# Kernel tuning notes

Hardware: AMD Instinct MI355X
Metric: run time of the kernel (lower is better)

## Reference

```python
import jax, jax.numpy as jnp
import numpy as np

MAX_DEG = 6

def _lookup(atoms, edges, maskvalue, include_self):
    # atoms: (B,N,F); edges: (B,N,D) with -1 padding. Shift indices by +1 and
    # prepend a mask row so padded slots read `maskvalue` (NGFP lookup_neighbors).
    B, N, F = atoms.shape
    pad = jnp.full((B, 1, F), maskvalue, atoms.dtype)
    padded = jnp.concatenate([pad, atoms], axis=1)          # (B,N+1,F)
    g = jax.vmap(lambda a, e: a[e])(padded, edges + 1)       # (B,N,D,F)
    if include_self:
        g = jnp.concatenate([atoms[:, :, None, :], g], axis=2)  # (B,N,D+1,F)
    return g

def _conv(atoms, bonds, edges, W, b):
    # Degree-specific dense layers, masked-summed (Duvenaud graph conv).
    deg = (edges != -1).sum(-1)                               # (B,N)
    summed = _lookup(atoms, edges, 0.0, True).sum(2)          # self + neighbors
    feat = jnp.concatenate([summed, bonds.sum(2)], axis=-1)   # (B,N,in)
    new = jax.nn.relu(jnp.einsum('bni,dio->bdno', feat, W) + b[None, :, None, :])
    m = (deg[:, None, :] == jnp.arange(MAX_DEG)[None, :, None]).astype(new.dtype)
    return jnp.einsum('bdno,bdn->bno', new, m)

def _pool(atoms, edges):
    nbr = _lookup(atoms, edges, -jnp.inf, True)
    mx = nbr.max(2)
    mask = ((edges != -1).sum(-1, keepdims=True) > 0).astype(atoms.dtype)
    return mx * mask

def _gout(atoms, bonds, edges, W, b):
    mask = ((edges != -1).sum(-1, keepdims=True) > 0).astype(atoms.dtype)
    feat = jnp.concatenate([atoms, bonds.sum(2)], axis=-1)
    fp = jnp.tanh(feat @ W + b) * mask
    return fp.sum(1)                                          # (B,H) graph fingerprint

def setup_inputs() -> dict:
    B, N, D = 2048, 60, MAX_DEG
    ATOM_F, BOND_F, H, C = 37, 6, 128, 12
    key = jax.random.key(0)
    ks = jax.random.split(key, 8)
    atoms = jax.random.normal(ks[0], (B, N, ATOM_F), jnp.float32)
    bonds = jax.random.uniform(ks[1], (B, N, D, BOND_F), jnp.float32)
    deg = jax.random.randint(ks[2], (B, N, 1), 1, 6)          # 1..5 neighbors per atom
    slot = jnp.arange(D)[None, None, :]
    nbrs = jax.random.randint(ks[3], (B, N, D), 0, N)
    edges = jnp.where(slot < deg, nbrs, -1)                   # -1 = padding
    s = lambda f: (2.0 / f) ** 0.5
    W1 = jax.random.normal(ks[4], (D, ATOM_F + BOND_F, H), jnp.float32) * s(ATOM_F + BOND_F)
    b1 = jnp.zeros((D, H), jnp.float32)
    W2 = jax.random.normal(ks[5], (D, H + BOND_F, H), jnp.float32) * s(H + BOND_F)
    b2 = jnp.zeros((D, H), jnp.float32)
    Wo = jax.random.normal(ks[6], (H + BOND_F, H), jnp.float32) * s(H + BOND_F)
    bo = jnp.zeros((H,), jnp.float32)
    Wfc = jax.random.normal(ks[7], (H, C), jnp.float32) * s(H)
    bfc = jnp.zeros((C,), jnp.float32)
    return dict(atoms=atoms, bonds=bonds, edges=edges, W1=W1, b1=b1,
                W2=W2, b2=b2, Wo=Wo, bo=bo, Wfc=Wfc, bfc=bfc)

def reference(atoms, bonds, edges, W1, b1, W2, b2, Wo, bo, Wfc, bfc):
    x = _conv(atoms, bonds, edges, W1, b1)   # gcn1
    x = _pool(x, edges)
    x = _conv(x, bonds, edges, W2, b2)       # gcn2
    x = _pool(x, edges)
    fp = _gout(x, bonds, edges, Wo, bo)      # graph output aggregation
    return jax.nn.sigmoid(fp @ Wfc + bfc)    # (B, n_class)
```

## Files before the change

kernel.cpp:

```cpp
#include <hip/hip_runtime.h>
#include <math.h>

typedef unsigned short u16;
typedef unsigned int   u32;
typedef unsigned long long u64;
typedef short  v8s __attribute__((ext_vector_type(8)));
typedef float  v4f __attribute__((ext_vector_type(4)));

constexpr int NB=2048, NN=60, DD=6, AF=37, BFD=6, HH=128, CC=12;
constexpr int T = 512;
constexpr int FASTR = 168;
constexpr int XSTR  = 132;
constexpr int KS1 = 2;
constexpr int KS2 = 5;
constexpr int MAXP = 32;

constexpr int W1T_UNITS = 6*8*KS1;
constexpr int W2T_UNITS = 6*8*KS2;
constexpr int WOT_UNITS = 8*KS2;
constexpr int TOT_UNITS = W1T_UNITS + W2T_UNITS + WOT_UNITS;
constexpr int W2T_OFF = W1T_UNITS*512;
constexpr int WOT_OFF = (W1T_UNITS+W2T_UNITS)*512;
constexpr int LO_OFF  = TOT_UNITS*512;

__device__ __forceinline__ u16 f2bf(float f) {
  u32 u = __float_as_uint(f);
  return (u16)((u + 0x7FFFu + ((u >> 16) & 1u)) >> 16);
}
__device__ __forceinline__ float bf2f(u16 h) { return __uint_as_float((u32)h << 16); }

__device__ __forceinline__ void split2(float a, float b, u32& hi, u32& lo) {
  u16 ha = f2bf(a), hb = f2bf(b);
  u32 la = __float_as_uint(a - bf2f(ha)) >> 16;
  u32 lb = __float_as_uint(b - bf2f(hb)) >> 16;
  hi = ((u32)hb << 16) | ha;
  lo = (lb << 16) | la;
}
__device__ __forceinline__ void split8(const float* v, uint4& hi, uint4& lo) {
  split2(v[0], v[1], hi.x, lo.x); split2(v[2], v[3], hi.y, lo.y);
  split2(v[4], v[5], hi.z, lo.z); split2(v[6], v[7], hi.w, lo.w);
}
__device__ __forceinline__ float fast_tanh(float x) {
  float e = __expf(2.f * x);
  return 1.f - 2.f / (e + 1.f);
}

__global__ __launch_bounds__(256) void prep_kernel(
    const float* __restrict__ W1, const float* __restrict__ W2,
    const float* __restrict__ Wo, u16* __restrict__ ws)
{
  int tid = blockIdx.x*256 + threadIdx.x;
  if (tid >= TOT_UNITS*512) return;
  int unit = tid >> 9, idx = tid & 511;
  int lane = idx >> 3, j = idx & 7;
  int n16 = lane & 15, q = lane >> 4;
  const float* src; int K, nt, ks;
  if (unit < W1T_UNITS) {
    int d = unit / 16, rem = unit % 16; nt = rem >> 1; ks = rem & 1;
    src = W1 + (size_t)d*43*128; K = 43;
  } else if (unit < W1T_UNITS + W2T_UNITS) {
    int u = unit - W1T_UNITS; int d = u / 40, rem = u % 40; nt = rem / 5; ks = rem % 5;
    src = W2 + (size_t)d*134*128; K = 134;
  } else {
    int u = unit - (W1T_UNITS + W2T_UNITS); nt = u / 5; ks = u % 5;
    src = Wo; K = 134;
  }
  int k = ks*32 + q*8 + j, n = nt*16 + n16;
  float v = (k < K) ? src[(size_t)k*128 + n] : 0.f;
  u16 hi = f2bf(v);
  u16 lo = (u16)(__float_as_uint(v - bf2f(hi)) >> 16);
  ws[(size_t)unit*512 + lane*8 + j] = hi;
  ws[(size_t)(LO_OFF + unit*512) + lane*8 + j] = lo;
}

template<int KSTEPS>
__device__ __forceinline__ void conv_mfma(
    const u16* __restrict__ wsW, const float* __restrict__ bias,
    const u16* sFA, float* sXout,
    const int* sSorted, const int* sDeg,
    const int* sPairD, const int* sPairM, int nP,
    int wv, int lane)
{
  const int n16 = lane & 15, q = lane >> 4;
  for (int u = wv; u < nP*4; u += 8) {
    const int p = u >> 2, nt0 = (u & 3) * 2;
    const int d = sPairD[p], mt = sPairM[p];
    const int row = mt*16 + n16;
    int nodes[4];
    #pragma unroll
    for (int r = 0; r < 4; ++r) nodes[r] = sSorted[mt*16 + q*4 + r];
    if (d == 6) {
      #pragma unroll 1
      for (int nt = nt0; nt < nt0+2; ++nt) {
        const int h = nt*16 + n16;
        #pragma unroll
        for (int r = 0; r < 4; ++r)
          if (nodes[r] >= 0 && sDeg[nodes[r]] == 6) sXout[nodes[r]*XSTR + h] = 0.f;
      }
      continue;
    }
    v8s ah[KSTEPS], al[KSTEPS];
    #pragma unroll
    for (int ks = 0; ks < KSTEPS; ++ks) {
      ah[ks] = *(const v8s*)(&sFA[row*FASTR + ks*32 + q*8]);
      al[ks] = *(const v8s*)(&sFA[(64 + row)*FASTR + ks*32 + q*8]);
    }
    #pragma unroll
    for (int nt = nt0; nt < nt0+2; ++nt) {
      v8s bh[KSTEPS], bl[KSTEPS];
      #pragma unroll
      for (int ks = 0; ks < KSTEPS; ++ks) {
        const size_t ub = ((size_t)((d*8 + nt)*KSTEPS + ks))*512;
        bh[ks] = ((const v8s*)(wsW + ub))[lane];
        bl[ks] = ((const v8s*)(wsW + LO_OFF + ub))[lane];
      }
      v4f acc = {0.f, 0.f, 0.f, 0.f};
      #pragma unroll
      for (int ks = 0; ks < KSTEPS; ++ks) {
        acc = __builtin_amdgcn_mfma_f32_16x16x32_bf16(ah[ks], bh[ks], acc, 0, 0, 0);
        acc = __builtin_amdgcn_mfma_f32_16x16x32_bf16(al[ks], bh[ks], acc, 0, 0, 0);
        acc = __builtin_amdgcn_mfma_f32_16x16x32_bf16(ah[ks], bl[ks], acc, 0, 0, 0);
      }
      const int h = nt*16 + n16;
      const float bb = bias[d*128 + h];
      #pragma unroll
      for (int r = 0; r < 4; ++r) {
        int node = nodes[r];
        if (node >= 0 && sDeg[node] == d)
          sXout[node*XSTR + h] = fmaxf(acc[r] + bb, 0.f);
      }
    }
  }
}

__global__ __launch_bounds__(T, 4) void ngfp_kernel(
    const float* __restrict__ atoms, const float* __restrict__ bonds,
    const int*   __restrict__ edges,
    const float* __restrict__ b1, const float* __restrict__ b2,
    const float* __restrict__ bo,
    const float* __restrict__ Wfc, const float* __restrict__ bfc,
    const u16*   __restrict__ ws,
    float* __restrict__ out)
{
  __shared__ u16   sFA[128*FASTR];
  __shared__ float sXa[NN*XSTR];
  __shared__ float sBsum[NN*BFD];
  __shared__ int  sEdges[NN*DD];
  __shared__ int  sDeg[NN];
  __shared__ int  sSorted[64];
  __shared__ int  sPairD[MAXP];
  __shared__ int  sPairM[MAXP];
  __shared__ int  sNP;
  __shared__ float sPart[HH];
  __shared__ float sRed[96];

  float* const sAtoms = sXa;

  const int b = blockIdx.x;
  const int t = threadIdx.x;
  const int wv = t >> 6;
  const int lane = t & 63;

  for (int i = t; i < NN*DD; i += T) sEdges[i] = edges[b*NN*DD + i];
  for (int i = t; i < NN*AF; i += T) sAtoms[i] = atoms[b*NN*AF + i];
  for (int i = t; i < NN*BFD; i += T) {
    int n = i / BFD, f = i - n*BFD;
    const float* bp = bonds + ((size_t)(b*NN + n)*DD)*BFD + f;
    float s = 0.f;
    #pragma unroll
    for (int d = 0; d < DD; ++d) s += bp[d*BFD];
    sBsum[i] = s;
  }
  __syncthreads();

  if (wv == 0) {
    const int n = lane;
    int dg = 7;
    if (n < NN) {
      dg = 0;
      #pragma unroll
      for (int d = 0; d < DD; ++d) dg += (sEdges[n*DD + d] != -1) ? 1 : 0;
      sDeg[n] = dg;
    } else {
      sSorted[n] = -1;
    }
    const u64 below = (lane == 63) ? ~0ull >> 1 : ((1ull << lane) - 1);
    int rs = 0, np = 0;
    #pragma unroll 1
    for (int d = 0; d < 7; ++d) {
      u64 m = __ballot(dg == d);
      int cnt = (int)__popcll(m);
      if (dg == d) sSorted[rs + (int)__popcll(m & below)] = n;
      if (lane == 0 && cnt > 0) {
        const int r1 = rs + cnt;
        for (int mt = rs >> 4; mt < ((r1 + 15) >> 4); ++mt) {
          sPairD[np] = d; sPairM[np] = mt; ++np;
        }
      }
      rs += cnt;
    }
    if (lane == 0) sNP = np;
  }
  __syncthreads();
  const int nP = sNP;

  {
    const int row = t >> 3, c = t & 7;
    const int node = sSorted[row];
    float acc[8] = {0,0,0,0,0,0,0,0};
    if (node >= 0) {
      int e[DD];
      #pragma unroll
      for (int d = 0; d < DD; ++d) e[d] = sEdges[node*DD + d];
      #pragma unroll
      for (int j = 0; j < 8; ++j) {
        int k = c*8 + j;
        float v = 0.f;
        if (k < AF) {
          v = sAtoms[node*AF + k];
          #pragma unroll
          for (int d = 0; d < DD; ++d) if (e[d] >= 0) v += sAtoms[e[d]*AF + k];
        } else if (k < AF + BFD) {
          v = sBsum[node*BFD + (k - AF)];
        }
        acc[j] = v;
      }
    }
    uint4 hi, lo; split8(acc, hi, lo);
    *(uint4*)(&sFA[row*FASTR + c*8]) = hi;
    *(uint4*)(&sFA[(64 + row)*FASTR + c*8]) = lo;
  }
  __syncthreads();

  conv_mfma<KS1>(ws, b1, sFA, sXa, sSorted, sDeg, sPairD, sPairM, nP, wv, lane);
  __syncthreads();

  {
    float4 m[4];
    #pragma unroll
    for (int j = 0; j < 4; ++j) {
      int idx = t + j*T;
      if (idx < NN*32) {
        int n = idx >> 5, c = idx & 31;
        float4 v = {0.f, 0.f, 0.f, 0.f};
        if (sDeg[n] > 0) {
          v = *(const float4*)(&sXa[n*XSTR + c*4]);
          #pragma unroll
          for (int d = 0; d < DD; ++d) {
            int e = sEdges[n*DD + d];
            if (e >= 0) {
              float4 u = *(const float4*)(&sXa[e*XSTR + c*4]);
              v.x = fmaxf(v.x, u.x); v.y = fmaxf(v.y, u.y);
              v.z = fmaxf(v.z, u.z); v.w = fmaxf(v.w, u.w);
            }
          }
        }
        m[j] = v;
      }
    }
    __syncthreads();
    #pragma unroll
    for (int j = 0; j < 4; ++j) {
      int idx = t + j*T;
      if (idx < NN*32) {
        int n = idx >> 5, c = idx & 31;
        *(float4*)(&sXa[n*XSTR + c*4]) = m[j];
      }
    }
  }
  __syncthreads();

  for (int unit = t; unit < 64*16; unit += T) {
    int row = unit >> 4, c = unit & 15;
    int node = sSorted[row];
    float acc[8] = {0,0,0,0,0,0,0,0};
    if (node >= 0) {
      *(float4*)(&acc[0]) = *(const float4*)(&sXa[node*XSTR + c*8]);
      *(float4*)(&acc[4]) = *(const float4*)(&sXa[node*XSTR + c*8 + 4]);
      #pragma unroll
      for (int d = 0; d < DD; ++d) {
        int e = sEdges[node*DD + d];
        if (e >= 0) {
          float4 u0 = *(const float4*)(&sXa[e*XSTR + c*8]);
          float4 u1 = *(const float4*)(&sXa[e*XSTR + c*8 + 4]);
          acc[0]+=u0.x; acc[1]+=u0.y; acc[2]+=u0.z; acc[3]+=u0.w;
          acc[4]+=u1.x; acc[5]+=u1.y; acc[6]+=u1.z; acc[7]+=u1.w;
        }
      }
    }
    uint4 hi, lo; split8(acc, hi, lo);
    *(uint4*)(&sFA[row*FASTR + c*8]) = hi;
    *(uint4*)(&sFA[(64 + row)*FASTR + c*8]) = lo;
  }
  if (t < 256) {
    int row = t >> 2, part = t & 3;
    uint4 hi = {0,0,0,0}, lo = {0,0,0,0};
    if (part == 0) {
      int node = sSorted[row];
      float acc[8] = {0,0,0,0,0,0,0,0};
      if (node >= 0) {
        #pragma unroll
        for (int j = 0; j < BFD; ++j) acc[j] = sBsum[node*BFD + j];
      }
      split8(acc, hi, lo);
    }
    *(uint4*)(&sFA[row*FASTR + 128 + part*8]) = hi;
    *(uint4*)(&sFA[(64 + row)*FASTR + 128 + part*8]) = lo;
  }
  __syncthreads();

  conv_mfma<KS2>(ws + W2T_OFF, b2, sFA, sXa, sSorted, sDeg, sPairD, sPairM, nP, wv, lane);
  __syncthreads();

  v8s g_bh[KS2], g_bl[KS2];
  {
    const int nt = wv;
    #pragma unroll
    for (int ks = 0; ks < KS2; ++ks) {
      const size_t ub = WOT_OFF + ((size_t)(nt*KS2 + ks))*512;
      g_bh[ks] = ((const v8s*)(ws + ub))[lane];
      g_bl[ks] = ((const v8s*)(ws + LO_OFF + ub))[lane];
    }
  }

  for (int unit = t; unit < 64*16; unit += T) {
    int row = unit >> 4, c = unit & 15;
    int node = sSorted[row];
    float acc[8] = {0,0,0,0,0,0,0,0};
    if (node >= 0 && sDeg[node] > 0) {
      float4 a0 = *(const float4*)(&sXa[node*XSTR + c*8]);
      float4 a1 = *(const float4*)(&sXa[node*XSTR + c*8 + 4]);
      #pragma unroll
      for (int d = 0; d < DD; ++d) {
        int e = sEdges[node*DD + d];
        if (e >= 0) {
          float4 u0 = *(const float4*)(&sXa[e*XSTR + c*8]);
          float4 u1 = *(const float4*)(&sXa[e*XSTR + c*8 + 4]);
          a0.x = fmaxf(a0.x, u0.x); a0.y = fmaxf(a0.y, u0.y);
          a0.z = fmaxf(a0.z, u0.z); a0.w = fmaxf(a0.w, u0.w);
          a1.x = fmaxf(a1.x, u1.x); a1.y = fmaxf(a1.y, u1.y);
          a1.z = fmaxf(a1.z, u1.z); a1.w = fmaxf(a1.w, u1.w);
        }
      }
      acc[0]=a0.x; acc[1]=a0.y; acc[2]=a0.z; acc[3]=a0.w;
      acc[4]=a1.x; acc[5]=a1.y; acc[6]=a1.z; acc[7]=a1.w;
    }
    uint4 hi, lo; split8(acc, hi, lo);
    *(uint4*)(&sFA[row*FASTR + c*8]) = hi;
    *(uint4*)(&sFA[(64 + row)*FASTR + c*8]) = lo;
  }
  __syncthreads();

  {
    const int nt = wv, n16 = lane & 15, q = lane >> 4;
    const int h = nt*16 + n16;
    const float bb = bo[h];
    float part = 0.f;
    #pragma unroll 2
    for (int mt = 0; mt < 4; ++mt) {
      const int row = mt*16 + n16;
      v4f acc = {0.f, 0.f, 0.f, 0.f};
      #pragma unroll
      for (int ks = 0; ks < KS2; ++ks) {
        v8s ah = *(const v8s*)(&sFA[row*FASTR + ks*32 + q*8]);
        v8s al = *(const v8s*)(&sFA[(64 + row)*FASTR + ks*32 + q*8]);
        acc = __builtin_amdgcn_mfma_f32_16x16x32_bf16(ah, g_bh[ks], acc, 0, 0, 0);
        acc = __builtin_amdgcn_mfma_f32_16x16x32_bf16(al, g_bh[ks], acc, 0, 0, 0);
        acc = __builtin_amdgcn_mfma_f32_16x16x32_bf16(ah, g_bl[ks], acc, 0, 0, 0);
      }
      #pragma unroll
      for (int r = 0; r < 4; ++r) {
        int node = sSorted[mt*16 + q*4 + r];
        if (node >= 0 && sDeg[node] > 0) part += fast_tanh(acc[r] + bb);
      }
    }
    part += __shfl_xor(part, 16);
    part += __shfl_xor(part, 32);
    if (lane < 16) sPart[h] = part;
  }
  __syncthreads();

  if (t < 96) {
    const int c = t >> 3, s = t & 7;
    float acc = 0.f;
    #pragma unroll
    for (int i = 0; i < 16; ++i) {
      int ii = s*16 + i;
      acc = fmaf(sPart[ii], Wfc[ii*CC + c], acc);
    }
    sRed[t] = acc;
  }
  __syncthreads();
  if (t < CC) {
    float acc = bfc[t];
    #pragma unroll
    for (int s = 0; s < 8; ++s) acc += sRed[t*8 + s];
    out[b*CC + t] = 1.f / (1.f + __expf(-acc));
  }
}

extern "C" void kernel_launch(void* const* d_in, const int* in_sizes, int n_in,
                              void* d_out, int out_size, void* d_ws, size_t ws_size,
                              hipStream_t stream) {
  const float* atoms = (const float*)d_in[0];
  const float* bonds = (const float*)d_in[1];
  const int*   edges = (const int*)d_in[2];
  const float* W1  = (const float*)d_in[3];
  const float* b1  = (const float*)d_in[4];
  const float* W2  = (const float*)d_in[5];
  const float* b2  = (const float*)d_in[6];
  const float* Wo  = (const float*)d_in[7];
  const float* bo  = (const float*)d_in[8];
  const float* Wfc = (const float*)d_in[9];
  const float* bfc = (const float*)d_in[10];
  float* out = (float*)d_out;
  u16* ws = (u16*)d_ws;

  prep_kernel<<<(TOT_UNITS*512 + 255)/256, 256, 0, stream>>>(W1, W2, Wo, ws);
  ngfp_kernel<<<NB, T, 0, stream>>>(atoms, bonds, edges, b1, b2, bo, Wfc, bfc, ws, out);
}
```

Before: 242.6 us.

## Double block size to 1024 threads and redistribute per-stage work across 16 waves

Raises the block to 1024 threads (16 waves) and re-partitions every stage to match. Feature gather/split now handles 4 columns per thread, pool loops run fewer iterations, and the output MFMA stage splits the four row tiles across two wave halves, with partial sums reduced through a doubled shared buffer. The aim is more in-flight waves per molecule to hide LDS and MFMA latency and shorten per-thread serial work. The tighter launch bound (8 waves per EU) caps registers per thread and may cause spills in the MFMA conv loop.

```diff
diff --git a/kernel.cpp b/kernel.cpp
--- a/kernel.cpp
+++ b/kernel.cpp
@@ -8,7 +8,8 @@
 typedef float  v4f __attribute__((ext_vector_type(4)));
 
 constexpr int NB=2048, NN=60, DD=6, AF=37, BFD=6, HH=128, CC=12;
-constexpr int T = 512;
+constexpr int T  = 1024;
+constexpr int NW = T/64;
 constexpr int FASTR = 168;
 constexpr int XSTR  = 132;
 constexpr int KS1 = 2;
@@ -39,6 +40,9 @@
 __device__ __forceinline__ void split8(const float* v, uint4& hi, uint4& lo) {
   split2(v[0], v[1], hi.x, lo.x); split2(v[2], v[3], hi.y, lo.y);
   split2(v[4], v[5], hi.z, lo.z); split2(v[6], v[7], hi.w, lo.w);
+}
+__device__ __forceinline__ void split4(const float* v, uint2& hi, uint2& lo) {
+  split2(v[0], v[1], hi.x, lo.x); split2(v[2], v[3], hi.y, lo.y);
 }
 __device__ __forceinline__ float fast_tanh(float x) {
   float e = __expf(2.f * x);
@@ -82,7 +86,7 @@
     int wv, int lane)
 {
   const int n16 = lane & 15, q = lane >> 4;
-  for (int u = wv; u < nP*4; u += 8) {
+  for (int u = wv; u < nP*4; u += NW) {
     const int p = u >> 2, nt0 = (u & 3) * 2;
     const int d = sPairD[p], mt = sPairM[p];
     const int row = mt*16 + n16;
@@ -133,7 +137,7 @@
   }
 }
 
-__global__ __launch_bounds__(T, 4) void ngfp_kernel(
+__global__ __launch_bounds__(T, 8) void ngfp_kernel(
     const float* __restrict__ atoms, const float* __restrict__ bonds,
     const int*   __restrict__ edges,
     const float* __restrict__ b1, const float* __restrict__ b2,
@@ -151,7 +155,7 @@
   __shared__ int  sPairD[MAXP];
   __shared__ int  sPairM[MAXP];
   __shared__ int  sNP;
-  __shared__ float sPart[HH];
+  __shared__ float sPart[2*HH];
   __shared__ float sRed[96];
 
   float* const sAtoms = sXa;
@@ -205,16 +209,16 @@
   const int nP = sNP;
 
   {
-    const int row = t >> 3, c = t & 7;
+    const int row = t >> 4, c = t & 15;
     const int node = sSorted[row];
-    float acc[8] = {0,0,0,0,0,0,0,0};
+    float acc[4] = {0,0,0,0};
     if (node >= 0) {
       int e[DD];
       #pragma unroll
       for (int d = 0; d < DD; ++d) e[d] = sEdges[node*DD + d];
       #pragma unroll
-      for (int j = 0; j < 8; ++j) {
-        int k = c*8 + j;
+      for (int j = 0; j < 4; ++j) {
+        int k = c*4 + j;
         float v = 0.f;
         if (k < AF) {
           v = sAtoms[node*AF + k];
@@ -226,9 +230,9 @@
         acc[j] = v;
       }
     }
-    uint4 hi, lo; split8(acc, hi, lo);
-    *(uint4*)(&sFA[row*FASTR + c*8]) = hi;
-    *(uint4*)(&sFA[(64 + row)*FASTR + c*8]) = lo;
+    uint2 hi, lo; split4(acc, hi, lo);
+    *(uint2*)(&sFA[row*FASTR + c*4]) = hi;
+    *(uint2*)(&sFA[(64 + row)*FASTR + c*4]) = lo;
   }
   __syncthreads();
 
@@ -236,9 +240,9 @@
   __syncthreads();
 
   {
-    float4 m[4];
-    #pragma unroll
-    for (int j = 0; j < 4; ++j) {
+    float4 m[2];
+    #pragma unroll
+    for (int j = 0; j < 2; ++j) {
       int idx = t + j*T;
       if (idx < NN*32) {
         int n = idx >> 5, c = idx & 31;
@@ -260,7 +264,7 @@
     }
     __syncthreads();
     #pragma unroll
-    for (int j = 0; j < 4; ++j) {
+    for (int j = 0; j < 2; ++j) {
       int idx = t + j*T;
       if (idx < NN*32) {
         int n = idx >> 5, c = idx & 31;
@@ -270,9 +274,9 @@
   }
   __syncthreads();
 
-  for (int unit = t; unit < 64*16; unit += T) {
-    int row = unit >> 4, c = unit & 15;
-    int node = sSorted[row];
+  {
+    const int row = t >> 4, c = t & 15;
+    const int node = sSorted[row];
     float acc[8] = {0,0,0,0,0,0,0,0};
     if (node >= 0) {
       *(float4*)(&acc[0]) = *(const float4*)(&sXa[node*XSTR + c*8]);
@@ -314,7 +318,7 @@
 
   v8s g_bh[KS2], g_bl[KS2];
   {
-    const int nt = wv;
+    const int nt = wv & 7;
     #pragma unroll
     for (int ks = 0; ks < KS2; ++ks) {
       const size_t ub = WOT_OFF + ((size_t)(nt*KS2 + ks))*512;
@@ -323,9 +327,9 @@
     }
   }
 
-  for (int unit = t; unit < 64*16; unit += T) {
-    int row = unit >> 4, c = unit & 15;
-    int node = sSorted[row];
+  {
+    const int row = t >> 4, c = t & 15;
+    const int node = sSorted[row];
     float acc[8] = {0,0,0,0,0,0,0,0};
     if (node >= 0 && sDeg[node] > 0) {
       float4 a0 = *(const float4*)(&sXa[node*XSTR + c*8]);
@@ -352,12 +356,14 @@
   __syncthreads();
 
   {
-    const int nt = wv, n16 = lane & 15, q = lane >> 4;
+    const int nt = wv & 7, half = wv >> 3;
+    const int n16 = lane & 15, q = lane >> 4;
     const int h = nt*16 + n16;
     const float bb = bo[h];
     float part = 0.f;
-    #pragma unroll 2
-    for (int mt = 0; mt < 4; ++mt) {
+    #pragma unroll
+    for (int mi = 0; mi < 2; ++mi) {
+      const int mt = half*2 + mi;
       const int row = mt*16 + n16;
       v4f acc = {0.f, 0.f, 0.f, 0.f};
       #pragma unroll
@@ -376,7 +382,7 @@
     }
     part += __shfl_xor(part, 16);
     part += __shfl_xor(part, 32);
-    if (lane < 16) sPart[h] = part;
+    if (lane < 16) sPart[half*HH + h] = part;
   }
   __syncthreads();
 
@@ -386,7 +392,7 @@
     #pragma unroll
     for (int i = 0; i < 16; ++i) {
       int ii = s*16 + i;
-      acc = fmaf(sPart[ii], Wfc[ii*CC + c], acc);
+      acc = fmaf(sPart[ii] + sPart[HH + ii], Wfc[ii*CC + c], acc);
     }
     sRed[t] = acc;
   }
```

Result: slower. 297.7 us (+22.7%).
